# Kernel tuning notes

Hardware: AMD Instinct MI355X
Metric: run time of the kernel (lower is better)

Reference implementation:

```python
import jax, jax.numpy as jnp
import numpy as np

N_TOKENS = 3
EMBED = 10
RNN = 10
N_LABELS = 3
B = 16384
T = 99
EPS = 1e-7  # keras CategoricalCrossentropy clip epsilon


def setup_inputs() -> dict:
    key = jax.random.key(0)
    ks = jax.random.split(key, 8)
    token_ids = jax.random.randint(ks[0], (B, T), 0, N_TOKENS, dtype=jnp.int32)
    label_ids = jax.random.randint(ks[1], (B, T), 0, N_LABELS)
    labels = jax.nn.one_hot(label_ids, N_LABELS, dtype=jnp.float32)
    mask = jnp.ones((B, T), dtype=bool)  # accepted by call() but unused, kept for signature fidelity
    emb_table = jax.random.normal(ks[2], (N_TOKENS, EMBED), jnp.float32) * 0.05
    W = jax.random.normal(ks[3], (EMBED, RNN), jnp.float32) / np.sqrt(EMBED)
    U = jax.random.normal(ks[4], (RNN, RNN), jnp.float32) / np.sqrt(RNN)
    b = jnp.zeros((RNN,), jnp.float32)
    Wo = jax.random.normal(ks[5], (RNN, N_LABELS), jnp.float32) / np.sqrt(RNN)
    bo = jnp.zeros((N_LABELS,), jnp.float32)
    return dict(token_ids=token_ids, labels=labels, mask=mask,
                emb_table=emb_table, W=W, U=U, b=b, Wo=Wo, bo=bo)


def reference(token_ids, labels, mask, emb_table, W, U, b, Wo, bo):
    # Embedding lookup (mask_zero=True -> token 0 is a masked step)
    emb = emb_table[token_ids]                      # [B, T, E]
    step_mask = (token_ids != 0)                    # [B, T]

    def step(h, inp):
        x_t, m_t = inp                              # [B, E], [B]
        h_new = jnp.tanh(x_t @ W + h @ U + b)       # SimpleRNN cell
        # Keras masking: masked timesteps carry previous state/output
        h = jnp.where(m_t[:, None], h_new, h)
        return h, h

    h0 = jnp.zeros((token_ids.shape[0], W.shape[1]), emb.dtype)
    _, states_tb = jax.lax.scan(step, h0, (emb.transpose(1, 0, 2), step_mask.T))
    states = states_tb.transpose(1, 0, 2)           # [B, T, R]

    probs = jax.nn.softmax(states @ Wo + bo, axis=-1)   # Dense(softmax) -> [B, T, L]
    probs_c = jnp.clip(probs, EPS, 1.0)
    loss = jnp.mean(-jnp.sum(labels * jnp.log(probs_c), axis=-1))
    accuracy = jnp.mean((jnp.argmax(probs, axis=-1) == jnp.argmax(labels, axis=-1)).astype(jnp.float32))
    return states, probs, accuracy, loss
```

## Files before the change

### kernel.cpp

```cpp
#include <hip/hip_runtime.h>
#include <math.h>

#define BB 16384
#define TT 99
#define RR 10
#define LL 3

#define QP(v, j) __int_as_float(__builtin_amdgcn_mov_dpp(                     \
    __float_as_int(v), (j) * 0x55, 0xF, 0xF, true))
#define HMIR(v)  __int_as_float(__builtin_amdgcn_mov_dpp(                     \
    __float_as_int(v), 0x141, 0xF, 0xF, true))

__device__ __forceinline__ void gather10(float hoA, float hoB, float (&hg)[RR]) {
    hg[0] = QP(hoA, 0); hg[1] = QP(hoA, 1);
    hg[2] = QP(hoA, 2); hg[3] = QP(hoA, 3);
    const float mr = HMIR(hoA);
    hg[4] = QP(mr, 0);  hg[5] = QP(mr, 1);
    hg[6] = QP(mr, 2);  hg[7] = QP(mr, 3);
    hg[8] = QP(hoB, 0); hg[9] = QP(hoB, 1);
}

__device__ __forceinline__ void epi_step(
    const float (&hg)[RR], int yv, int tep, int g,
    const float (&Wc)[RR], float boc,
    float* __restrict__ prow, float& loss, int& corr)
{
    float lg = boc;
#pragma unroll
    for (int i = 0; i < RR; ++i) lg = fmaf(hg[i], Wc[i], lg);
    const float eo = __expf(lg);
    const float e0 = QP(eo, 0), e1 = QP(eo, 1), e2 = QP(eo, 2);
    const float S  = e0 + e1 + e2;
    const float rs = __builtin_amdgcn_rcpf(S);
    if (g < 3) prow[tep * LL + g] = eo * rs;

    const float ey = (yv == 0) ? e0 : ((yv == 1) ? e1 : e2);
    const float py = fmaxf(ey * rs, 1e-7f);
    const float lt = -__logf(py);

    int ap = 0; float pm = e0;
    if (e1 > pm) { ap = 1; pm = e1; }
    if (e2 > pm) { ap = 2; }
    if (g == 0) { loss += lt; corr += (ap == yv) ? 1 : 0; }
}

template <int TB, int N>
__device__ __forceinline__ void rnn_section(
    uint64_t wsel, uint64_t wy, float& hoA, float& hoB,
    const float (&UA)[RR], const float (&UB)[RR],
    const float (&Wc)[RR], float boc,
    float cA1, float cA2, float cB1, float cB2,
    float* __restrict__ outA, float* __restrict__ outB,
    float* __restrict__ prow, int g, float& loss, int& corr)
{
#pragma unroll
    for (int u = 0; u < N; ++u) {
        const int sel = (int)(wsel & 3); wsel >>= 2;
        const int yv  = (int)(wy & 3);   wy >>= 2;

        float hg[RR];
        gather10(hoA, hoB, hg);

        if (TB + u > 0)
            epi_step(hg, yv, TB + u - 1, g, Wc, boc, prow, loss, corr);

        const bool is1 = (sel == 1);
        float aA0 = is1 ? cA1 : cA2, aB0 = is1 ? cB1 : cB2;
        float aA1 = 0.0f, aB1 = 0.0f;
#pragma unroll
        for (int i = 0; i < 5; ++i) {
            aA0 = fmaf(hg[i],     UA[i],     aA0);
            aA1 = fmaf(hg[5 + i], UA[5 + i], aA1);
            aB0 = fmaf(hg[i],     UB[i],     aB0);
            aB1 = fmaf(hg[5 + i], UB[5 + i], aB1);
        }
        const float eA = __expf(2.0f * (aA0 + aA1));
        const float eB = __expf(2.0f * (aB0 + aB1));
        const float pA = eA + 1.0f, pB = eB + 1.0f;
        const float r  = __builtin_amdgcn_rcpf(pA * pB);
        const float hnA = fmaf(-2.0f * pB, r, 1.0f);
        const float hnB = fmaf(-2.0f * pA, r, 1.0f);
        if (sel != 0) { hoA = hnA; hoB = hnB; }

        outA[(TB + u) * RR] = hoA;
        outB[(TB + u) * RR] = hoB;
    }
}

__global__ __launch_bounds__(256, 2)
void rnn_fused_kernel(const int* __restrict__ tok_ids,
                      const float* __restrict__ labels,
                      const float* __restrict__ emb,
                      const float* __restrict__ W,
                      const float* __restrict__ U,
                      const float* __restrict__ bvec,
                      const float* __restrict__ Wo,
                      const float* __restrict__ bo,
                      float* __restrict__ states_out,
                      float* __restrict__ probs_out,
                      float* __restrict__ ws)
{
    __shared__ unsigned char s_code[4][8 * 100];

    const int tid = threadIdx.x;
    const int w   = tid >> 6;
    const int l   = tid & 63;
    const int r8  = l >> 3;
    const int g   = l & 7;
    const int rowbase = blockIdx.x * 32 + w * 8;

#pragma unroll
    for (int i = 0; i < 13; ++i) {
        const int p = l + 64 * i;
        if (p < 8 * TT) {
            const size_t gi = (size_t)rowbase * TT + p;
            const int   tk  = tok_ids[gi];
            const float la1 = labels[gi * LL + 1];
            const float la2 = labels[gi * LL + 2];
            const int   y   = (la1 > 0.5f) ? 1 : ((la2 > 0.5f) ? 2 : 0);
            const int   r   = p / TT;
            s_code[w][r * 100 + (p - r * TT)] = (unsigned char)((tk << 2) | y);
        }
    }

    const unsigned char* cp = &s_code[w][r8 * 100];
    uint64_t sw0 = 0, sw1 = 0, sw2 = 0, sw3 = 0;
    uint64_t yw0 = 0, yw1 = 0, yw2 = 0, yw3 = 0;
#pragma unroll
    for (int t = 0; t < TT; ++t) {
        const uint64_t c  = (uint64_t)cp[t];
        const uint64_t sv = (c >> 2) & 3, yv = c & 3;
        if (t < 32)              sw0 |= sv << (2 * t);
        else if (t < 64)         sw1 |= sv << (2 * (t - 32));
        else if (t < 96)         sw2 |= sv << (2 * (t - 64));
        else                     sw3 |= sv << (2 * (t - 96));
        const int s2 = t + 1;
        if (s2 < 32)             yw0 |= yv << (2 * s2);
        else if (s2 < 64)        yw1 |= yv << (2 * (s2 - 32));
        else if (s2 < 96)        yw2 |= yv << (2 * (s2 - 64));
        else                     yw3 |= yv << (2 * (s2 - 96));
    }
    const int y98 = (int)((yw3 >> 6) & 3);

    const int qpar = g >> 2;
    int ord[8];
#pragma unroll
    for (int j = 0; j < 4; ++j) {
        ord[j]     = qpar ? 4 + j : j;
        ord[4 + j] = qpar ? 3 - j : 7 - j;
    }
    const int jA = g;
    const int jB = ((g & 3) < 2) ? 8 + (g & 3) : 8;
    const int gc = ((g & 3) < 2) ? (g & 3) : 2;

    float UA[RR], UB[RR], Wc[RR];
#pragma unroll
    for (int k2 = 0; k2 < 8; ++k2) {
        UA[k2] = U[ord[k2] * RR + jA];
        UB[k2] = U[ord[k2] * RR + jB];
        Wc[k2] = Wo[ord[k2] * LL + gc];
    }
    UA[8] = U[8 * RR + jA]; UA[9] = U[9 * RR + jA];
    UB[8] = U[8 * RR + jB]; UB[9] = U[9 * RR + jB];
    Wc[8] = Wo[8 * LL + gc]; Wc[9] = Wo[9 * LL + gc];
    const float boc = bo[gc];

    float cA1 = bvec[jA], cA2 = cA1, cB1 = bvec[jB], cB2 = cB1;
#pragma unroll
    for (int i = 0; i < RR; ++i) {
        const float e1 = emb[RR + i];
        const float e2 = emb[2 * RR + i];
        const float wA = W[i * RR + jA];
        const float wB = W[i * RR + jB];
        cA1 = fmaf(e1, wA, cA1); cA2 = fmaf(e2, wA, cA2);
        cB1 = fmaf(e1, wB, cB1); cB2 = fmaf(e2, wB, cB2);
    }

    const int row = rowbase + r8;
    float* outA = states_out + (size_t)row * (TT * RR) + jA;
    float* outB = states_out + (size_t)row * (TT * RR) + jB;
    float* prow = probs_out  + (size_t)row * (TT * LL);

    float hoA = 0.0f, hoB = 0.0f;
    float loss = 0.0f;
    int   corr = 0;

    rnn_section< 0, 32>(sw0, yw0, hoA, hoB, UA, UB, Wc, boc,
                        cA1, cA2, cB1, cB2, outA, outB, prow, g, loss, corr);
    rnn_section<32, 32>(sw1, yw1, hoA, hoB, UA, UB, Wc, boc,
                        cA1, cA2, cB1, cB2, outA, outB, prow, g, loss, corr);
    rnn_section<64, 32>(sw2, yw2, hoA, hoB, UA, UB, Wc, boc,
                        cA1, cA2, cB1, cB2, outA, outB, prow, g, loss, corr);
    rnn_section<96,  3>(sw3, yw3, hoA, hoB, UA, UB, Wc, boc,
                        cA1, cA2, cB1, cB2, outA, outB, prow, g, loss, corr);

    {
        float hg[RR];
        gather10(hoA, hoB, hg);
        epi_step(hg, y98, 98, g, Wc, boc, prow, loss, corr);
    }

    float ls = loss, cs = (float)corr;
#pragma unroll
    for (int off = 32; off > 0; off >>= 1) {
        ls += __shfl_down(ls, off, 64);
        cs += __shfl_down(cs, off, 64);
    }
    if (l == 0) {
        const int wid = blockIdx.x * 4 + w;
        ws[wid]        = ls;
        ws[2048 + wid] = cs;
    }
}

__global__ __launch_bounds__(256)
void finalize_kernel(const float* __restrict__ ws, float* __restrict__ out_tail)
{
    __shared__ float sl[4], sc[4];
    const int t = threadIdx.x;
    float ls = 0.0f, cs = 0.0f;
#pragma unroll
    for (int i = 0; i < 8; ++i) {
        ls += ws[t + 256 * i];
        cs += ws[2048 + t + 256 * i];
    }
#pragma unroll
    for (int off = 32; off > 0; off >>= 1) {
        ls += __shfl_down(ls, off, 64);
        cs += __shfl_down(cs, off, 64);
    }
    if ((t & 63) == 0) { sl[t >> 6] = ls; sc[t >> 6] = cs; }
    __syncthreads();
    if (t == 0) {
        const float L = sl[0] + sl[1] + sl[2] + sl[3];
        const float C = sc[0] + sc[1] + sc[2] + sc[3];
        const float inv = 1.0f / (float)((size_t)BB * TT);
        out_tail[0] = C * inv;
        out_tail[1] = L * inv;
    }
}

extern "C" void kernel_launch(void* const* d_in, const int* in_sizes, int n_in,
                              void* d_out, int out_size, void* d_ws, size_t ws_size,
                              hipStream_t stream)
{
    const int*   tok    = (const int*)  d_in[0];
    const float* labels = (const float*)d_in[1];
    const float* emb = (const float*)d_in[3];
    const float* W   = (const float*)d_in[4];
    const float* U   = (const float*)d_in[5];
    const float* bv  = (const float*)d_in[6];
    const float* Wo  = (const float*)d_in[7];
    const float* bo  = (const float*)d_in[8];

    float* out    = (float*)d_out;
    float* states = out;
    float* probs  = out + (size_t)BB * TT * RR;
    float* tail   = out + (size_t)BB * TT * (RR + LL);
    float* ws     = (float*)d_ws;

    rnn_fused_kernel<<<BB / 32, 256, 0, stream>>>(tok, labels, emb, W, U, bv,
                                                  Wo, bo, states, probs, ws);
    finalize_kernel<<<1, 256, 0, stream>>>(ws, tail);
}
```

Before: 57.44 us.

## Split softmax, loss and accuracy out of the RNN recurrence into a separate kernel

The recurrent kernel now only writes raw logits, with the label index packed into the low two mantissa bits of logit 0. A new grid-stride kernel reads those logits back, computes the softmax, the clipped cross-entropy via log-sum-exp and the argmax accuracy, then writes block partials for the finalize step. The aim is to take the exp, reciprocal, log and DPP shuffles off the serial recurrence critical path and run them in a fully parallel pass. In exchange the probs buffer is read and written a second time, a kernel launch is added, and the packed label bits slightly perturb logit 0.

```diff
diff --git a/kernel.cpp b/kernel.cpp
--- a/kernel.cpp
+++ b/kernel.cpp
@@ -20,28 +20,15 @@
     hg[8] = QP(hoB, 0); hg[9] = QP(hoB, 1);
 }
 
-__device__ __forceinline__ void epi_step(
+__device__ __forceinline__ void logit_step(
     const float (&hg)[RR], int yv, int tep, int g,
-    const float (&Wc)[RR], float boc,
-    float* __restrict__ prow, float& loss, int& corr)
+    const float (&Wc)[RR], float boc, float* __restrict__ prow)
 {
     float lg = boc;
 #pragma unroll
     for (int i = 0; i < RR; ++i) lg = fmaf(hg[i], Wc[i], lg);
-    const float eo = __expf(lg);
-    const float e0 = QP(eo, 0), e1 = QP(eo, 1), e2 = QP(eo, 2);
-    const float S  = e0 + e1 + e2;
-    const float rs = __builtin_amdgcn_rcpf(S);
-    if (g < 3) prow[tep * LL + g] = eo * rs;
-
-    const float ey = (yv == 0) ? e0 : ((yv == 1) ? e1 : e2);
-    const float py = fmaxf(ey * rs, 1e-7f);
-    const float lt = -__logf(py);
-
-    int ap = 0; float pm = e0;
-    if (e1 > pm) { ap = 1; pm = e1; }
-    if (e2 > pm) { ap = 2; }
-    if (g == 0) { loss += lt; corr += (ap == yv) ? 1 : 0; }
+    if (g == 0) lg = __int_as_float((__float_as_int(lg) & ~3) | yv);
+    if (g < 3) prow[tep * LL + g] = lg;
 }
 
 template <int TB, int N>
@@ -51,7 +38,7 @@
     const float (&Wc)[RR], float boc,
     float cA1, float cA2, float cB1, float cB2,
     float* __restrict__ outA, float* __restrict__ outB,
-    float* __restrict__ prow, int g, float& loss, int& corr)
+    float* __restrict__ prow, int g)
 {
 #pragma unroll
     for (int u = 0; u < N; ++u) {
@@ -62,7 +49,7 @@
         gather10(hoA, hoB, hg);
 
         if (TB + u > 0)
-            epi_step(hg, yv, TB + u - 1, g, Wc, boc, prow, loss, corr);
+            logit_step(hg, yv, TB + u - 1, g, Wc, boc, prow);
 
         const bool is1 = (sel == 1);
         float aA0 = is1 ? cA1 : cA2, aB0 = is1 ? cB1 : cB2;
@@ -88,17 +75,16 @@
 }
 
 __global__ __launch_bounds__(256, 2)
-void rnn_fused_kernel(const int* __restrict__ tok_ids,
-                      const float* __restrict__ labels,
-                      const float* __restrict__ emb,
-                      const float* __restrict__ W,
-                      const float* __restrict__ U,
-                      const float* __restrict__ bvec,
-                      const float* __restrict__ Wo,
-                      const float* __restrict__ bo,
-                      float* __restrict__ states_out,
-                      float* __restrict__ probs_out,
-                      float* __restrict__ ws)
+void rnn_seq_kernel(const int* __restrict__ tok_ids,
+                    const float* __restrict__ labels,
+                    const float* __restrict__ emb,
+                    const float* __restrict__ W,
+                    const float* __restrict__ U,
+                    const float* __restrict__ bvec,
+                    const float* __restrict__ Wo,
+                    const float* __restrict__ bo,
+                    float* __restrict__ states_out,
+                    float* __restrict__ logits_out)
 {
     __shared__ unsigned char s_code[4][8 * 100];
 
@@ -179,37 +165,69 @@
     const int row = rowbase + r8;
     float* outA = states_out + (size_t)row * (TT * RR) + jA;
     float* outB = states_out + (size_t)row * (TT * RR) + jB;
-    float* prow = probs_out  + (size_t)row * (TT * LL);
+    float* prow = logits_out + (size_t)row * (TT * LL);
 
     float hoA = 0.0f, hoB = 0.0f;
-    float loss = 0.0f;
-    int   corr = 0;
 
     rnn_section< 0, 32>(sw0, yw0, hoA, hoB, UA, UB, Wc, boc,
-                        cA1, cA2, cB1, cB2, outA, outB, prow, g, loss, corr);
+                        cA1, cA2, cB1, cB2, outA, outB, prow, g);
     rnn_section<32, 32>(sw1, yw1, hoA, hoB, UA, UB, Wc, boc,
-                        cA1, cA2, cB1, cB2, outA, outB, prow, g, loss, corr);
+                        cA1, cA2, cB1, cB2, outA, outB, prow, g);
     rnn_section<64, 32>(sw2, yw2, hoA, hoB, UA, UB, Wc, boc,
-                        cA1, cA2, cB1, cB2, outA, outB, prow, g, loss, corr);
+                        cA1, cA2, cB1, cB2, outA, outB, prow, g);
     rnn_section<96,  3>(sw3, yw3, hoA, hoB, UA, UB, Wc, boc,
-                        cA1, cA2, cB1, cB2, outA, outB, prow, g, loss, corr);
+                        cA1, cA2, cB1, cB2, outA, outB, prow, g);
 
     {
         float hg[RR];
         gather10(hoA, hoB, hg);
-        epi_step(hg, y98, 98, g, Wc, boc, prow, loss, corr);
-    }
-
+        logit_step(hg, y98, 98, g, Wc, boc, prow);
+    }
+}
+
+__global__ __launch_bounds__(256)
+void softmax_kernel(float* __restrict__ probs,
+                    float* __restrict__ ws)
+{
+    const int NT     = BB * TT;
+    const int tid    = blockIdx.x * 256 + threadIdx.x;
+    const int stride = 2048 * 256;
+
+    float loss = 0.0f;
+    int   corr = 0;
+
+#pragma unroll 1
+    for (int idx = tid; idx < NT; idx += stride) {
+        float* pp = probs + (size_t)idx * LL;
+        const float l0 = pp[0], l1 = pp[1], l2 = pp[2];
+        const int   y  = __float_as_int(l0) & 3;
+
+        const float e0 = __expf(l0), e1 = __expf(l1), e2 = __expf(l2);
+        const float S  = e0 + e1 + e2;
+        const float rs = __builtin_amdgcn_rcpf(S);
+        pp[0] = e0 * rs; pp[1] = e1 * rs; pp[2] = e2 * rs;
+
+        const float ly = (y == 0) ? l0 : ((y == 1) ? l1 : l2);
+        loss += fminf(__logf(S) - ly, 16.11809565f);
+
+        int ap = 0; float pm = l0;
+        if (l1 > pm) { ap = 1; pm = l1; }
+        if (l2 > pm) { ap = 2; }
+        corr += (ap == y) ? 1 : 0;
+    }
+
+    __shared__ float sl[4], sc[4];
     float ls = loss, cs = (float)corr;
 #pragma unroll
     for (int off = 32; off > 0; off >>= 1) {
         ls += __shfl_down(ls, off, 64);
         cs += __shfl_down(cs, off, 64);
     }
-    if (l == 0) {
-        const int wid = blockIdx.x * 4 + w;
-        ws[wid]        = ls;
-        ws[2048 + wid] = cs;
+    if ((threadIdx.x & 63) == 0) { sl[threadIdx.x >> 6] = ls; sc[threadIdx.x >> 6] = cs; }
+    __syncthreads();
+    if (threadIdx.x == 0) {
+        ws[blockIdx.x]        = sl[0] + sl[1] + sl[2] + sl[3];
+        ws[2048 + blockIdx.x] = sc[0] + sc[1] + sc[2] + sc[3];
     }
 }
 
@@ -259,7 +277,8 @@
     float* tail   = out + (size_t)BB * TT * (RR + LL);
     float* ws     = (float*)d_ws;
 
-    rnn_fused_kernel<<<BB / 32, 256, 0, stream>>>(tok, labels, emb, W, U, bv,
-                                                  Wo, bo, states, probs, ws);
+    rnn_seq_kernel<<<BB / 32, 256, 0, stream>>>(tok, labels, emb, W, U, bv,
+                                                Wo, bo, states, probs);
+    softmax_kernel<<<2048, 256, 0, stream>>>(probs, ws);
     finalize_kernel<<<1, 256, 0, stream>>>(ws, tail);
 }
```

After: 52.98 us. 1.08x faster.
